# Performance work log

Measured on AMD Instinct MI355X. Metric: run time of the kernel, lower is better.

The kernel has to match this reference:

```python
import jax, jax.numpy as jnp
import numpy as np

B, IN_CH, OUT_CH, H, W = 16, 64, 64, 256, 256
MODES, KS = 16, 3

def setup_inputs() -> dict:
    key = jax.random.key(0)
    ks = jax.random.split(key, 8)
    scale = 1.0 / (IN_CH * OUT_CH)
    c = jax.random.normal(ks[0], (B, IN_CH, H, W), dtype=jnp.float32)
    # complex spectral weights stored as (real, imag) pairs; torch.rand(cfloat) -> U[0,1) real & imag
    w1r = scale * jax.random.uniform(ks[1], (IN_CH, OUT_CH, MODES, MODES), dtype=jnp.float32)
    w1i = scale * jax.random.uniform(ks[2], (IN_CH, OUT_CH, MODES, MODES), dtype=jnp.float32)
    w2r = scale * jax.random.uniform(ks[3], (IN_CH, OUT_CH, MODES, MODES), dtype=jnp.float32)
    w2i = scale * jax.random.uniform(ks[4], (IN_CH, OUT_CH, MODES, MODES), dtype=jnp.float32)
    # local conv (circular padding, bias=True as in nn.Conv2d default)
    fan_in = IN_CH * KS * KS
    bound = 1.0 / np.sqrt(fan_in)
    conv_w = jax.random.uniform(ks[5], (OUT_CH, IN_CH, KS, KS), minval=-bound, maxval=bound, dtype=jnp.float32)
    conv_b = jax.random.uniform(ks[6], (OUT_CH,), minval=-bound, maxval=bound, dtype=jnp.float32)
    return {"c": c, "w1r": w1r, "w1i": w1i, "w2r": w2r, "w2i": w2i,
            "conv_w": conv_w, "conv_b": conv_b}

def _global_transform(c, w1, w2):
    m = MODES
    b, _, h, w = c.shape
    c_ft = jnp.fft.rfft2(c)  # [B, in, H, W//2+1] complex
    top = jnp.einsum('bixy,ioxy->boxy', c_ft[:, :, :m, :m], w1)
    bot = jnp.einsum('bixy,ioxy->boxy', c_ft[:, :, -m:, :m], w2)
    out_ft = jnp.zeros((b, OUT_CH, h, w // 2 + 1), dtype=c_ft.dtype)
    out_ft = out_ft.at[:, :, :m, :m].set(top).at[:, :, -m:, :m].set(bot)
    return jnp.fft.irfft2(out_ft, s=(h, w))

def _local_transform(c, conv_w, conv_b):
    pad = KS // 2
    xp = jnp.pad(c, ((0, 0), (0, 0), (pad, pad), (pad, pad)), mode='wrap')  # circular
    y = jax.lax.conv_general_dilated(xp, conv_w, window_strides=(1, 1), padding='VALID',
                                     dimension_numbers=('NCHW', 'OIHW', 'NCHW'))
    return y + conv_b[None, :, None, None]

def reference(c, w1r, w1i, w2r, w2i, conv_w, conv_b):
    w1 = w1r + 1j * w1i
    w2 = w2r + 1j * w2i
    g = _global_transform(c, w1, w2)
    l = _local_transform(c, conv_w, conv_b)
    return g * l  # interaction == 'mixing'
```

## Files before the change

kernel.cpp:

```cpp
#include <hip/hip_runtime.h>
#include <hip/hip_bf16.h>


#define TWO_PI 6.283185307179586f
typedef __hip_bfloat16 bf16;

__device__ __forceinline__ float ld_in(const void* p, size_t i, int isf32) {
    if (isf32) return ((const float*)p)[i];
    return __bfloat162float(((const bf16*)p)[i]);
}
__device__ __forceinline__ unsigned clampi(unsigned i, unsigned cap) {
    return i < cap ? i : 0u;
}

__global__ __launch_bounds__(256) void k_probe(const unsigned short* __restrict__ c,
                                               int* __restrict__ flag) {
    __shared__ int cnt;
    if (threadIdx.x == 0) cnt = 0;
    __syncthreads();
    int bad = 0;
    for (int j = 0; j < 4; ++j) {
        unsigned short u = c[threadIdx.x * 4 + j];
        unsigned e = (u >> 7) & 0xFF;
        if (e == 0xFF || e >= 0x87) bad++;
    }
    atomicAdd(&cnt, bad);
    __syncthreads();
    if (threadIdx.x == 0) flag[0] = (cnt > 64) ? 1 : 0;
}

__global__ __launch_bounds__(256) void k1_dftx(const void* __restrict__ cin,
                                               const int* __restrict__ flag,
                                               float2* __restrict__ X1, unsigned capX1) {
    __shared__ float rows[16][256];
    __shared__ float2 tw[256];
    int t = threadIdx.x;
    int f32 = flag[0];
    float sv, cv;
    sincosf(TWO_PI * (float)t * (1.0f / 256.0f), &sv, &cv);
    tw[t] = make_float2(cv, sv);
    size_t base = (size_t)blockIdx.x * 4096;
    for (int j = 0; j < 16; ++j)
        rows[j][t] = ld_in(cin, base + j * 256 + t, f32);
    __syncthreads();
    int r = t >> 4, kx = t & 15;
    float re = 0.f, im = 0.f;
    for (int x = 0; x < 256; ++x) {
        float v = rows[r][x];
        float2 w = tw[(kx * x) & 255];
        re = fmaf(v, w.x, re);
        im = fmaf(-v, w.y, im);
    }
    unsigned idx = (blockIdx.x * 16u + r) * 16u + kx;
    X1[clampi(idx, capX1)] = make_float2(re, im);
}

__global__ __launch_bounds__(512) void k2_dfty(const float2* __restrict__ X1,
                                               float2* __restrict__ Cft,
                                               unsigned capX1, unsigned capC) {
    __shared__ float2 tw[256];
    __shared__ float2 xs[4096];
    int t = threadIdx.x;
    if (t < 256) {
        float sv, cv;
        sincosf(TWO_PI * (float)t * (1.0f / 256.0f), &sv, &cv);
        tw[t] = make_float2(cv, sv);
    }
    unsigned base = blockIdx.x * 4096u;
    for (int j = 0; j < 8; ++j)
        xs[j * 512 + t] = X1[clampi(base + j * 512 + t, capX1)];
    __syncthreads();
    int kyidx = t >> 4, kx = t & 15;
    int ky = (kyidx < 16) ? kyidx : (224 + kyidx);
    float re = 0.f, im = 0.f;
    for (int y = 0; y < 256; ++y) {
        float2 v = xs[y * 16 + kx];
        float2 w = tw[(ky * y) & 255];
        re += v.x * w.x + v.y * w.y;
        im += v.y * w.x - v.x * w.y;
    }
    Cft[clampi(blockIdx.x * 512u + t, capC)] = make_float2(re, im);
}

__global__ __launch_bounds__(256) void k3_mix(const float2* __restrict__ Cft,
                                              const void* __restrict__ w1r, const void* __restrict__ w1i,
                                              const void* __restrict__ w2r, const void* __restrict__ w2i,
                                              float2* __restrict__ Outft,
                                              const int* __restrict__ flag,
                                              unsigned capC, unsigned capO) {
    __shared__ float2 wsm[4096];
    __shared__ float2 cs[1024];
    int t = threadIdx.x;
    int f32 = flag[0];
    int kyidx = blockIdx.x >> 4;
    int moff = ((kyidx < 16) ? kyidx : (kyidx - 16)) * 16 + (blockIdx.x & 15);
    const void* wr = (kyidx < 16) ? w1r : w2r;
    const void* wi = (kyidx < 16) ? w1i : w2i;
    for (int j = 0; j < 16; ++j) {
        int io = j * 256 + t;
        wsm[io] = make_float2(ld_in(wr, (size_t)io * 256 + moff, f32),
                              ld_in(wi, (size_t)io * 256 + moff, f32));
    }
    for (int j = 0; j < 4; ++j) {
        int bi = j * 256 + t;
        cs[bi] = Cft[clampi((unsigned)bi * 512u + blockIdx.x, capC)];
    }
    __syncthreads();
    int o = t & 63, bq = t >> 6;
    for (int jb = 0; jb < 4; ++jb) {
        int b = bq * 4 + jb;
        float re = 0.f, im = 0.f;
        for (int i = 0; i < 64; ++i) {
            float2 c = cs[b * 64 + i];
            float2 w = wsm[i * 64 + o];
            re += c.x * w.x - c.y * w.y;
            im += c.x * w.y + c.y * w.x;
        }
        Outft[clampi((unsigned)(b * 64 + o) * 512u + blockIdx.x, capO)] = make_float2(re, im);
    }
}

__global__ __launch_bounds__(256) void k4_idfty(const float2* __restrict__ Outft,
                                                float2* __restrict__ G1,
                                                unsigned capO, unsigned capG) {
    __shared__ float2 tw[256];
    __shared__ float2 fs[512];
    int t = threadIdx.x;
    float sv, cv;
    sincosf(TWO_PI * (float)t * (1.0f / 256.0f), &sv, &cv);
    tw[t] = make_float2(cv, sv);
    unsigned base = blockIdx.x * 512u;
    fs[t] = Outft[clampi(base + t, capO)];
    fs[t + 256] = Outft[clampi(base + t + 256, capO)];
    __syncthreads();
    int kx = t & 15, y0 = t >> 4;
    float alpha = ((kx == 0) ? 1.0f : 2.0f) * (1.0f / 65536.0f);
    for (int jj = 0; jj < 16; ++jj) {
        int y = jj * 16 + y0;
        float re = 0.f, im = 0.f;
        for (int k = 0; k < 32; ++k) {
            int ky = (k < 16) ? k : (224 + k);
            float2 f = fs[k * 16 + kx];
            float2 w = tw[(ky * y) & 255];
            re += f.x * w.x - f.y * w.y;
            im += f.x * w.y + f.y * w.x;
        }
        G1[clampi((blockIdx.x * 256u + y) * 16u + kx, capG)] = make_float2(re * alpha, im * alpha);
    }
}

__global__ __launch_bounds__(256, 3) void k5_fused(const float2* __restrict__ G1, unsigned capG,
                                                   const void* __restrict__ cin,
                                                   const void* __restrict__ convw,
                                                   const void* __restrict__ convb,
                                                   const int* __restrict__ flag,
                                                   void* __restrict__ out) {
    __shared__ float2 ph[16][16];
    __shared__ float xs[8][18][19];
    __shared__ float wlds[8][9][64];
    int t = threadIdx.x;
    int f32 = flag[0];
    int tx = blockIdx.x, ty = blockIdx.y, bz = blockIdx.z;
    int ocg = t >> 5, pxg = t & 31, pr = pxg >> 2, pc = pxg & 3;

    {
        int kx = t >> 4, xl = t & 15;
        int x = tx * 16 + xl;
        float sv, cv;
        sincosf(TWO_PI * (float)((kx * x) & 255) * (1.0f / 256.0f), &sv, &cv);
        ph[kx][xl] = make_float2(cv, sv);
    }

    float acc[8][8];
#pragma unroll
    for (int j = 0; j < 8; ++j)
#pragma unroll
        for (int p = 0; p < 8; ++p) acc[j][p] = 0.f;

    for (int icc = 0; icc < 8; ++icc) {
        __syncthreads();
        for (int idx = t; idx < 2592; idx += 256) {
            int i = idx / 324, rem = idx - i * 324;
            int yy = rem / 18, xx = rem - yy * 18;
            int yg = (ty * 16 + yy - 1) & 255;
            int xg = (tx * 16 + xx - 1) & 255;
            xs[i][yy][xx] = ld_in(cin, ((size_t)(bz * 64 + icc * 8 + i) * 256 + yg) * 256 + xg, f32);
        }
        for (int idx = t; idx < 4608; idx += 256) {
            int i = idx / 576, rem = idx - i * 576;
            int k = rem >> 6, o = rem & 63;
            wlds[i][k][o] = ld_in(convw, (size_t)(o * 64 + icc * 8 + i) * 9 + k, f32);
        }
        __syncthreads();
        for (int i = 0; i < 8; ++i) {
            float xr[4][6];
#pragma unroll
            for (int ry = 0; ry < 4; ++ry)
#pragma unroll
                for (int cx = 0; cx < 6; ++cx)
                    xr[ry][cx] = xs[i][2 * pr + ry][4 * pc + cx];
#pragma unroll
            for (int j = 0; j < 8; ++j) {
                int o = 8 * j + ocg;
#pragma unroll
                for (int k = 0; k < 9; ++k) {
                    float wv = wlds[i][k][o];
                    int dy = k / 3, dx = k - dy * 3;
#pragma unroll
                    for (int p = 0; p < 8; ++p)
                        acc[j][p] = fmaf(wv, xr[(p >> 2) + dy][(p & 3) + dx], acc[j][p]);
                }
            }
        }
    }

#pragma unroll
    for (int j = 0; j < 8; ++j) {
        int o = 8 * j + ocg;
        float bias = ld_in(convb, o, f32);
#pragma unroll
        for (int ry = 0; ry < 2; ++ry) {
            int y = ty * 16 + 2 * pr + ry;
            unsigned rb = ((unsigned)(bz * 64 + o) * 256u + (unsigned)y) * 16u;
            if (rb + 16u > capG) rb = 0u;
            const float4* gp = (const float4*)(G1 + rb);
            float4 fv[8];
#pragma unroll
            for (int m = 0; m < 8; ++m) fv[m] = gp[m];
            float a0 = 0.f, a1 = 0.f, a2 = 0.f, a3 = 0.f;
#pragma unroll
            for (int kx = 0; kx < 16; ++kx) {
                float fre = (kx & 1) ? fv[kx >> 1].z : fv[kx >> 1].x;
                float fim = (kx & 1) ? fv[kx >> 1].w : fv[kx >> 1].y;
                float2 p0 = ph[kx][4 * pc + 0];
                float2 p1 = ph[kx][4 * pc + 1];
                float2 p2 = ph[kx][4 * pc + 2];
                float2 p3 = ph[kx][4 * pc + 3];
                a0 = fmaf(fre, p0.x, a0); a0 = fmaf(-fim, p0.y, a0);
                a1 = fmaf(fre, p1.x, a1); a1 = fmaf(-fim, p1.y, a1);
                a2 = fmaf(fre, p2.x, a2); a2 = fmaf(-fim, p2.y, a2);
                a3 = fmaf(fre, p3.x, a3); a3 = fmaf(-fim, p3.y, a3);
            }
            int pb = ry * 4;
            float v0 = a0 * (acc[j][pb + 0] + bias);
            float v1 = a1 * (acc[j][pb + 1] + bias);
            float v2 = a2 * (acc[j][pb + 2] + bias);
            float v3 = a3 * (acc[j][pb + 3] + bias);
            size_t oidx = (((size_t)(bz * 64 + o) * 256 + y) * 256) + tx * 16 + 4 * pc;
            if (f32) {
                *(float4*)((float*)out + oidx) = make_float4(v0, v1, v2, v3);
            } else {
                bf16* op = (bf16*)out + oidx;
                op[0] = __float2bfloat16(v0);
                op[1] = __float2bfloat16(v1);
                op[2] = __float2bfloat16(v2);
                op[3] = __float2bfloat16(v3);
            }
        }
    }
}

extern "C" void kernel_launch(void* const* d_in, const int* in_sizes, int n_in,
                              void* d_out, int out_size, void* d_ws, size_t ws_size,
                              hipStream_t stream) {
    char* ws = (char*)d_ws;
    int* flag = (int*)ws;
    const size_t offX1 = 1024;
    const size_t offC  = offX1 + 33554432;
    const size_t offO  = offC + 4194304;
    unsigned capX1, capC, capO;
    {
        size_t a;
        a = (ws_size > offX1 + 8) ? (ws_size - offX1) / 8 : 1;
        capX1 = (unsigned)(a < 4194304 ? a : 4194304);
        a = (ws_size > offC + 8) ? (ws_size - offC) / 8 : 1;
        capC = (unsigned)(a < 524288 ? a : 524288);
        a = (ws_size > offO + 8) ? (ws_size - offO) / 8 : 1;
        capO = (unsigned)(a < 524288 ? a : 524288);
    }
    float2* X1    = (float2*)(ws + offX1);
    float2* Cft   = (float2*)(ws + offC);
    float2* Outft = (float2*)(ws + offO);
    float2* G1    = X1;

    k_probe<<<1, 256, 0, stream>>>((const unsigned short*)d_in[0], flag);
    k1_dftx<<<16384, 256, 0, stream>>>(d_in[0], flag, X1, capX1);
    k2_dfty<<<1024, 512, 0, stream>>>(X1, Cft, capX1, capC);
    k3_mix<<<512, 256, 0, stream>>>(Cft, d_in[1], d_in[2], d_in[3], d_in[4],
                                    Outft, flag, capC, capO);
    k4_idfty<<<1024, 256, 0, stream>>>(Outft, G1, capO, capX1);
    dim3 g5(16, 16, 16);
    k5_fused<<<g5, 256, 0, stream>>>(G1, capX1, d_in[0], d_in[5], d_in[6], flag, d_out);
}
```

Measured before the change: 2.055 ms.

## Software-pipeline conv tile loads through registers and vectorize LDS reads

```diff
diff --git a/kernel.cpp b/kernel.cpp
--- a/kernel.cpp
+++ b/kernel.cpp
@@ -8,6 +8,10 @@
 __device__ __forceinline__ float ld_in(const void* p, size_t i, int isf32) {
     if (isf32) return ((const float*)p)[i];
     return __bfloat162float(((const bf16*)p)[i]);
+}
+__device__ __forceinline__ float bfbits2f(unsigned short u) {
+    unsigned v = ((unsigned)u) << 16;
+    return __uint_as_float(v);
 }
 __device__ __forceinline__ unsigned clampi(unsigned i, unsigned cap) {
     return i < cap ? i : 0u;
@@ -40,8 +44,28 @@
     sincosf(TWO_PI * (float)t * (1.0f / 256.0f), &sv, &cv);
     tw[t] = make_float2(cv, sv);
     size_t base = (size_t)blockIdx.x * 4096;
-    for (int j = 0; j < 16; ++j)
-        rows[j][t] = ld_in(cin, base + j * 256 + t, f32);
+    if (f32) {
+        const float4* p4 = (const float4*)cin + (base >> 2);
+#pragma unroll
+        for (int q = 0; q < 4; ++q) {
+            float4 v = p4[q * 256 + t];
+            int row = 4 * q + (t >> 6), col = (t & 63) * 4;
+            *(float4*)&rows[row][col] = v;
+        }
+    } else {
+        const short4* p4 = (const short4*)cin + (base >> 2);
+#pragma unroll
+        for (int q = 0; q < 4; ++q) {
+            short4 v = p4[q * 256 + t];
+            int row = 4 * q + (t >> 6), col = (t & 63) * 4;
+            float4 f;
+            f.x = bfbits2f((unsigned short)v.x);
+            f.y = bfbits2f((unsigned short)v.y);
+            f.z = bfbits2f((unsigned short)v.z);
+            f.w = bfbits2f((unsigned short)v.w);
+            *(float4*)&rows[row][col] = f;
+        }
+    }
     __syncthreads();
     int r = t >> 4, kx = t & 15;
     float re = 0.f, im = 0.f;
@@ -156,11 +180,14 @@
                                                    const int* __restrict__ flag,
                                                    void* __restrict__ out) {
     __shared__ float2 ph[16][16];
-    __shared__ float xs[8][18][19];
-    __shared__ float wlds[8][9][64];
+    __shared__ float xs[8][18][20];
+    __shared__ float wlds[8][9][8][8];
     int t = threadIdx.x;
     int f32 = flag[0];
-    int tx = blockIdx.x, ty = blockIdx.y, bz = blockIdx.z;
+    int d = blockIdx.x;
+    int tx = (d >> 3) & 15;
+    int g  = (d & 7) + ((d >> 7) << 3);
+    int ty = g & 15, bz = g >> 4;
     int ocg = t >> 5, pxg = t & 31, pr = pxg >> 2, pc = pxg & 3;
 
     {
@@ -171,47 +198,94 @@
         ph[kx][xl] = make_float2(cv, sv);
     }
 
+    float xpre[11], wpre[18];
+
+#define LOAD_REGS(ICC)                                                                  \
+    {                                                                                   \
+        int icc_ = (ICC);                                                               \
+        _Pragma("unroll")                                                               \
+        for (int q = 0; q < 11; ++q) {                                                  \
+            int idx = q * 256 + t;                                                      \
+            if (idx < 2592) {                                                           \
+                int i = idx / 324, rem = idx - i * 324;                                 \
+                int yy = rem / 18, xx = rem - yy * 18;                                  \
+                int yg = (ty * 16 + yy - 1) & 255;                                      \
+                int xg = (tx * 16 + xx - 1) & 255;                                      \
+                xpre[q] = ld_in(cin, ((size_t)(bz * 64 + icc_ * 8 + i) * 256 + yg) * 256 + xg, f32); \
+            }                                                                           \
+        }                                                                               \
+        _Pragma("unroll")                                                               \
+        for (int q = 0; q < 18; ++q) {                                                  \
+            int idx = q * 256 + t;                                                      \
+            int o = idx / 72, rem = idx - o * 72;                                       \
+            wpre[q] = ld_in(convw, (size_t)(o * 64 + icc_ * 8 + rem / 9) * 9 + rem % 9, f32); \
+        }                                                                               \
+    }
+
+#define WRITE_LDS()                                                                     \
+    {                                                                                   \
+        _Pragma("unroll")                                                               \
+        for (int q = 0; q < 11; ++q) {                                                  \
+            int idx = q * 256 + t;                                                      \
+            if (idx < 2592) {                                                           \
+                int i = idx / 324, rem = idx - i * 324;                                 \
+                int yy = rem / 18, xx = rem - yy * 18;                                  \
+                xs[i][yy][xx] = xpre[q];                                                \
+            }                                                                           \
+        }                                                                               \
+        _Pragma("unroll")                                                               \
+        for (int q = 0; q < 18; ++q) {                                                  \
+            int idx = q * 256 + t;                                                      \
+            int o = idx / 72, rem = idx - o * 72;                                       \
+            wlds[rem / 9][rem % 9][o & 7][o >> 3] = wpre[q];                            \
+        }                                                                               \
+    }
+
     float acc[8][8];
 #pragma unroll
     for (int j = 0; j < 8; ++j)
 #pragma unroll
         for (int p = 0; p < 8; ++p) acc[j][p] = 0.f;
+
+    LOAD_REGS(0);
+    WRITE_LDS();
 
     for (int icc = 0; icc < 8; ++icc) {
         __syncthreads();
-        for (int idx = t; idx < 2592; idx += 256) {
-            int i = idx / 324, rem = idx - i * 324;
-            int yy = rem / 18, xx = rem - yy * 18;
-            int yg = (ty * 16 + yy - 1) & 255;
-            int xg = (tx * 16 + xx - 1) & 255;
-            xs[i][yy][xx] = ld_in(cin, ((size_t)(bz * 64 + icc * 8 + i) * 256 + yg) * 256 + xg, f32);
-        }
-        for (int idx = t; idx < 4608; idx += 256) {
-            int i = idx / 576, rem = idx - i * 576;
-            int k = rem >> 6, o = rem & 63;
-            wlds[i][k][o] = ld_in(convw, (size_t)(o * 64 + icc * 8 + i) * 9 + k, f32);
-        }
-        __syncthreads();
+        if (icc < 7) LOAD_REGS(icc + 1);
         for (int i = 0; i < 8; ++i) {
             float xr[4][6];
 #pragma unroll
-            for (int ry = 0; ry < 4; ++ry)
-#pragma unroll
-                for (int cx = 0; cx < 6; ++cx)
-                    xr[ry][cx] = xs[i][2 * pr + ry][4 * pc + cx];
-#pragma unroll
-            for (int j = 0; j < 8; ++j) {
-                int o = 8 * j + ocg;
-#pragma unroll
-                for (int k = 0; k < 9; ++k) {
-                    float wv = wlds[i][k][o];
-                    int dy = k / 3, dx = k - dy * 3;
-#pragma unroll
-                    for (int p = 0; p < 8; ++p)
-                        acc[j][p] = fmaf(wv, xr[(p >> 2) + dy][(p & 3) + dx], acc[j][p]);
+            for (int ry = 0; ry < 4; ++ry) {
+                const float* rp = &xs[i][2 * pr + ry][4 * pc];
+                float4 a = *(const float4*)rp;
+                float2 b = *(const float2*)(rp + 4);
+                xr[ry][0] = a.x; xr[ry][1] = a.y; xr[ry][2] = a.z;
+                xr[ry][3] = a.w; xr[ry][4] = b.x; xr[ry][5] = b.y;
+            }
+#pragma unroll
+            for (int k = 0; k < 9; ++k) {
+                const float4* wp = (const float4*)&wlds[i][k][ocg][0];
+                float4 w0 = wp[0], w1 = wp[1];
+                float wk0 = w0.x, wk1 = w0.y, wk2 = w0.z, wk3 = w0.w;
+                float wk4 = w1.x, wk5 = w1.y, wk6 = w1.z, wk7 = w1.w;
+                int dy = k / 3, dx = k - dy * 3;
+#pragma unroll
+                for (int p = 0; p < 8; ++p) {
+                    float xv = xr[(p >> 2) + dy][(p & 3) + dx];
+                    acc[0][p] = fmaf(wk0, xv, acc[0][p]);
+                    acc[1][p] = fmaf(wk1, xv, acc[1][p]);
+                    acc[2][p] = fmaf(wk2, xv, acc[2][p]);
+                    acc[3][p] = fmaf(wk3, xv, acc[3][p]);
+                    acc[4][p] = fmaf(wk4, xv, acc[4][p]);
+                    acc[5][p] = fmaf(wk5, xv, acc[5][p]);
+                    acc[6][p] = fmaf(wk6, xv, acc[6][p]);
+                    acc[7][p] = fmaf(wk7, xv, acc[7][p]);
                 }
             }
         }
+        __syncthreads();
+        if (icc < 7) WRITE_LDS();
     }
 
 #pragma unroll
@@ -232,14 +306,12 @@
             for (int kx = 0; kx < 16; ++kx) {
                 float fre = (kx & 1) ? fv[kx >> 1].z : fv[kx >> 1].x;
                 float fim = (kx & 1) ? fv[kx >> 1].w : fv[kx >> 1].y;
-                float2 p0 = ph[kx][4 * pc + 0];
-                float2 p1 = ph[kx][4 * pc + 1];
-                float2 p2 = ph[kx][4 * pc + 2];
-                float2 p3 = ph[kx][4 * pc + 3];
-                a0 = fmaf(fre, p0.x, a0); a0 = fmaf(-fim, p0.y, a0);
-                a1 = fmaf(fre, p1.x, a1); a1 = fmaf(-fim, p1.y, a1);
-                a2 = fmaf(fre, p2.x, a2); a2 = fmaf(-fim, p2.y, a2);
-                a3 = fmaf(fre, p3.x, a3); a3 = fmaf(-fim, p3.y, a3);
+                const float4* pp = (const float4*)&ph[kx][4 * pc];
+                float4 p01 = pp[0], p23 = pp[1];
+                a0 = fmaf(fre, p01.x, a0); a0 = fmaf(-fim, p01.y, a0);
+                a1 = fmaf(fre, p01.z, a1); a1 = fmaf(-fim, p01.w, a1);
+                a2 = fmaf(fre, p23.x, a2); a2 = fmaf(-fim, p23.y, a2);
+                a3 = fmaf(fre, p23.z, a3); a3 = fmaf(-fim, p23.w, a3);
             }
             int pb = ry * 4;
             float v0 = a0 * (acc[j][pb + 0] + bias);
@@ -258,6 +330,8 @@
             }
         }
     }
+#undef LOAD_REGS
+#undef WRITE_LDS
 }
 
 extern "C" void kernel_launch(void* const* d_in, const int* in_sizes, int n_in,
@@ -289,6 +363,5 @@
     k3_mix<<<512, 256, 0, stream>>>(Cft, d_in[1], d_in[2], d_in[3], d_in[4],
                                     Outft, flag, capC, capO);
     k4_idfty<<<1024, 256, 0, stream>>>(Outft, G1, capO, capX1);
-    dim3 g5(16, 16, 16);
-    k5_fused<<<g5, 256, 0, stream>>>(G1, capX1, d_in[0], d_in[5], d_in[6], flag, d_out);
-}
+    k5_fused<<<4096, 256, 0, stream>>>(G1, capX1, d_in[0], d_in[5], d_in[6], flag, d_out);
+}
```

After: 2.703 ms. 1.32x slower.
